# Performance work log

Hardware: AMD Instinct MI355X
Metric: run time of the kernel (lower is better)

The kernel has to match this reference:

```python
import jax, jax.numpy as jnp
import numpy as np

EPS = 1e-7
C_IN = 1.0
C_ATTN = 1.0
C_OUT = 1.0
B, N, D_IN, H, D_OUT = 4, 2048, 128, 8, 64  # in_features = D_IN+1, ambient A = D_OUT+1
INIT_BOUND = 0.02


def _lift(spatial, c):
    # lift spatial coords to hyperboloid of curvature c: x0 = sqrt(1/c + ||x_s||^2)
    time = jnp.sqrt(1.0 / c + jnp.sum(spatial * spatial, axis=-1, keepdims=True))
    return jnp.concatenate([time, spatial], axis=-1)


def _lorentz_normalize(mu, c):
    # project weighted sum back onto hyperboloid: mu / (sqrt(c) * sqrt(|<mu,mu>_L|))
    lor = -mu[..., 0:1] ** 2 + jnp.sum(mu[..., 1:] ** 2, axis=-1, keepdims=True)
    return mu / (jnp.sqrt(c) * jnp.sqrt(jnp.clip(-lor, EPS)))


def setup_inputs() -> dict:
    key = jax.random.key(0)
    ks = jax.random.split(key, 8)
    x_spatial = jax.random.normal(ks[0], (B, N, D_IN), dtype=jnp.float32) * 0.5
    x = _lift(x_spatial, C_IN)  # valid hyperboloid points, curvature C_IN
    u = lambda k, shp: jax.random.uniform(k, shp, minval=-INIT_BOUND, maxval=INIT_BOUND, dtype=jnp.float32)
    return {
        "x": x,
        "Wq": u(ks[1], (H, D_IN + 1, D_OUT)),
        "Wk": u(ks[2], (H, D_IN + 1, D_OUT)),
        "Wv": u(ks[3], (H, D_IN + 1, D_OUT)),
        "bq": u(ks[4], (H, D_OUT)),
        "bk": u(ks[5], (H, D_OUT)),
        "bv": u(ks[6], (H, D_OUT)),
        "scale": jnp.array(1.0, dtype=jnp.float32),
        "attn_bias": jnp.array(0.0, dtype=jnp.float32),
    }


def reference(x, Wq, Wk, Wv, bq, bk, bv, scale, attn_bias):
    # HTCLinear per head (vectorized over heads): spatial = x @ W + b, lift to curvature C_ATTN
    def proj(W, b):
        s = jnp.einsum('bni,hid->bnhd', x, W) + b  # (B,N,H,D_OUT)
        return _lift(s, C_ATTN)                    # (B,N,H,D_OUT+1)

    q = proj(Wq, bq)
    k = proj(Wk, bk)
    v = proj(Wv, bv)

    # Lorentzian inner product scores: -q0*k0 + q_s . k_s  -> (B,N,H,M)
    li = (-jnp.einsum('bnh,bmh->bnhm', q[..., 0], k[..., 0])
          + jnp.einsum('bnhd,bmhd->bnhm', q[..., 1:], k[..., 1:]))
    scores = (2.0 + 2.0 * li) / (scale + EPS) + attn_bias
    w = jax.nn.softmax(scores, axis=-1)

    # Lorentz midpoint aggregation over keys
    mu = jnp.einsum('bnhm,bmha->bnha', w, v)
    mid = _lorentz_normalize(mu, C_ATTN)  # (B,N,H,A)

    # uniform Lorentz midpoint over heads (weights 1/H)
    avg = jnp.mean(mid, axis=2)           # (B,N,A)
    out = _lorentz_normalize(avg, C_ATTN)

    # spatial_to_hyperboloid: rescale curvature C_ATTN -> C_OUT and re-lift
    spatial = out[..., 1:] * jnp.sqrt(C_ATTN / C_OUT)
    return _lift(spatial, C_OUT)  # (B,N,D_OUT+1)
```

## Files before the change

### kernel.cpp

```cpp
#include <hip/hip_runtime.h>
#include <hip/hip_bf16.h>

typedef __bf16 bf16x8 __attribute__((ext_vector_type(8)));
typedef float f32x16 __attribute__((ext_vector_type(16)));
typedef unsigned int u32;
typedef unsigned short u16;
typedef u32 u32x2 __attribute__((ext_vector_type(2)));
typedef u32 u32x4 __attribute__((ext_vector_type(4)));

static constexpr int Nn  = 2048;
static constexpr int DIN = 129;
static constexpr int QP  = 80;
static constexpr int AMB = 65;
static constexpr int XP  = 144;
static constexpr int NS  = 2;
static constexpr int PR  = 72;
static constexpr int KROW = 88;
static constexpr int KTS  = 3072;
static constexpr int VROW = 40;
static constexpr int VTS  = 4096;
static constexpr float LOG2E = 1.4426950408889634f;

#define DEV static __device__ __forceinline__

#if __has_builtin(__builtin_amdgcn_exp2f)
#define FEXP2 __builtin_amdgcn_exp2f
#else
#define FEXP2 exp2f
#endif

DEV u16 f2bf(float f) {
  union { __bf16 h; u16 u; } c;
  c.h = (__bf16)f;
  return c.u;
}
DEV float bf2f(u16 u) {
  union { float f; u32 uu; } c;
  c.uu = ((u32)u) << 16;
  return c.f;
}
DEV u32 cvtpk(float a, float b) {
  u32 r;
  asm("v_cvt_pk_bf16_f32 %0, %1, %2" : "=v"(r) : "v"(a), "v"(b));
  return r;
}
DEV void swap32(u32& a, u32& b) {
  asm("v_permlane32_swap_b32 %0, %1" : "+v"(a), "+v"(b));
}
DEV void gload_lds16(const u16* g, u16* l) {
  __builtin_amdgcn_global_load_lds(
      (const __attribute__((address_space(1))) unsigned int*)g,
      (__attribute__((address_space(3))) unsigned int*)l, 16, 0, 0);
}

__global__ __launch_bounds__(256) void prep_k(const float* __restrict__ x,
                                              u16* __restrict__ xb) {
  const int t = blockIdx.x * 256 + threadIdx.x;
  const int row = t / 18, cg = t % 18;
  u16 tmp[8];
#pragma unroll
  for (int j = 0; j < 8; ++j) {
    const int c = cg * 8 + j;
    tmp[j] = (c < DIN) ? f2bf(x[(size_t)row * DIN + c]) : (u16)0;
  }
  u32x4 w;
  w[0] = (u32)tmp[0] | ((u32)tmp[1] << 16);
  w[1] = (u32)tmp[2] | ((u32)tmp[3] << 16);
  w[2] = (u32)tmp[4] | ((u32)tmp[5] << 16);
  w[3] = (u32)tmp[6] | ((u32)tmp[7] << 16);
  *((u32x4*)xb + t) = w;
}

__global__ __launch_bounds__(256) void proj_k(
    const u16* __restrict__ xb,
    const float* __restrict__ Wq, const float* __restrict__ Wk, const float* __restrict__ Wv,
    const float* __restrict__ bq, const float* __restrict__ bk, const float* __restrict__ bv,
    const float* __restrict__ scale_p,
    u16* __restrict__ Qb, u16* __restrict__ Ktl, u16* __restrict__ Vtl) {
  __shared__ u16 wt[64][152];
  __shared__ __align__(16) u16 tiles[4][2816];

  const int tid = threadIdx.x;
  const int wid = tid >> 6, l = tid & 63;
  const int z = blockIdx.y;
  const int T = z >> 3, h = z & 7;
  const float* W    = (T == 0 ? Wq : (T == 1 ? Wk : Wv)) + (size_t)h * DIN * 64;
  const float* bias = (T == 0 ? bq : (T == 1 ? bk : bv)) + h * 64;

  {
    const int d = tid & 63, kk = tid >> 6;
    for (int k = kk; k < XP; k += 4)
      wt[d][k] = (k < DIN) ? f2bf(W[(size_t)k * 64 + d]) : (u16)0;
  }
  __syncthreads();

  const int lo = l & 31, hi = l >> 5;
  const int row0 = (blockIdx.x * 4 + wid) * 32;
  const u16* xr = xb + (size_t)(row0 + lo) * XP;

  f32x16 acc0 = {}, acc1 = {};
#pragma unroll
  for (int s = 0; s < 9; ++s) {
    bf16x8 a  = *(const bf16x8*)&xr[16 * s + 8 * hi];
    bf16x8 b0 = *(const bf16x8*)&wt[lo][16 * s + 8 * hi];
    bf16x8 b1 = *(const bf16x8*)&wt[32 + lo][16 * s + 8 * hi];
    acc0 = __builtin_amdgcn_mfma_f32_32x32x16_bf16(a, b0, acc0, 0, 0, 0);
    acc1 = __builtin_amdgcn_mfma_f32_32x32x16_bf16(a, b1, acc1, 0, 0, 0);
  }
  const float b0v = bias[lo], b1v = bias[32 + lo];
  const float alpha = 2.0f * LOG2E / (scale_p[0] + 1e-7f);
  u16* tl = &tiles[wid][0];

#pragma unroll
  for (int r = 0; r < 16; ++r) {
    const float s0 = acc0[r] + b0v;
    const float s1 = acc1[r] + b1v;
    float part = s0 * s0 + s1 * s1;
#pragma unroll
    for (int m = 1; m < 32; m <<= 1) part += __shfl_xor(part, m);
    const float time = sqrtf(1.0f + part);
    const int dr = (r & 3) + 8 * (r >> 2) + 4 * hi;
    if (T == 0) {
      tl[dr * 80 + lo]      = f2bf(alpha * s0);
      tl[dr * 80 + 32 + lo] = f2bf(alpha * s1);
      if (lo == 0) tl[dr * 80 + 64] = f2bf(alpha * time);
      if (lo < 15) tl[dr * 80 + 65 + lo] = 0;
    } else if (T == 1) {
      tl[dr * 88 + lo]      = f2bf(s0);
      tl[dr * 88 + 32 + lo] = f2bf(s1);
      if (lo == 0) tl[dr * 88 + 64] = f2bf(-(time - 1.0f));
      if (lo < 15) tl[dr * 88 + 65 + lo] = 0;
      if (lo < 8)  tl[dr * 88 + 80 + lo] = 0;
    } else {
      tl[lo * 40 + dr]        = f2bf(s0);
      tl[(32 + lo) * 40 + dr] = f2bf(s1);
      if (lo == 0) tl[64 * 40 + dr] = f2bf(time);
    }
  }
  __syncthreads();

  const int b = row0 >> 11, n0 = row0 & 2047;
  const int bh = b * 8 + h;
  u16* gdst;
  int nch;
  if (T == 0) { gdst = Qb + ((size_t)bh * Nn + n0) * QP;                nch = 320; }
  else if (T == 1) { gdst = Ktl + (size_t)bh * 64 * KTS + (size_t)(n0 >> 5) * KTS; nch = 352; }
  else { gdst = Vtl + (size_t)bh * 64 * VTS + (size_t)(n0 >> 5) * VTS;  nch = 325; }
  for (int j = l; j < nch; j += 64)
    *(u32x4*)(gdst + j * 8) = *(const u32x4*)(tl + j * 8);
}

DEV void stage_tile(const u16* kg, const u16* vg, u16* kl, u16* vl,
                    const int w, const int lane) {
  if (w < 2) {
#pragma unroll
    for (int i = 0; i < 3; ++i)
      gload_lds16(kg + (w * 3 + i) * 512 + lane * 8, kl + (w * 3 + i) * 512);
    gload_lds16(vg + w * 512 + lane * 8, vl + w * 512);
  } else {
#pragma unroll
    for (int i = 0; i < 3; ++i) {
      const int j = (w - 2) * 3 + 2 + i;
      gload_lds16(vg + j * 512 + lane * 8, vl + j * 512);
    }
  }
}

DEV void waitbar(const int w) {
  if (w < 2)
    asm volatile("s_waitcnt vmcnt(4) lgkmcnt(0)\ns_barrier" ::: "memory");
  else
    asm volatile("s_waitcnt vmcnt(3) lgkmcnt(0)\ns_barrier" ::: "memory");
}

DEV void exp_pack(const f32x16 sc, bf16x8& fA, bf16x8& fB) {
  float p[16];
#pragma unroll
  for (int r = 0; r < 16; ++r) p[r] = FEXP2(sc[r]);
  u32 a0 = cvtpk(p[0], p[1]),  a1 = cvtpk(p[2], p[3]);
  u32 a2 = cvtpk(p[4], p[5]),  a3 = cvtpk(p[6], p[7]);
  u32 c0 = cvtpk(p[8], p[9]),  c1 = cvtpk(p[10], p[11]);
  u32 c2 = cvtpk(p[12], p[13]), c3 = cvtpk(p[14], p[15]);
  swap32(a0, a2);
  swap32(a1, a3);
  swap32(c0, c2);
  swap32(c1, c3);
  union { u32x4 u; bf16x8 b; } ca, cb;
  ca.u = (u32x4){a0, a1, a2, a3};
  cb.u = (u32x4){c0, c1, c2, c3};
  fA = ca.b;
  fB = cb.b;
}

DEV void compute_tile64(const u16* kl, const u16* vl, const int lo, const int hi,
                        const bf16x8 (&qA)[5], const bf16x8 (&qB)[5],
                        f32x16& a0, f32x16& a1, f32x16& a2,
                        f32x16& b0, f32x16& b1, f32x16& b2) {
  f32x16 sA = {}, sB = {};
#pragma unroll
  for (int s = 0; s < 5; ++s) {
    const bf16x8 kf = *(const bf16x8*)&kl[lo * KROW + 16 * s + 8 * hi];
    sA = __builtin_amdgcn_mfma_f32_32x32x16_bf16(kf, qA[s], sA, 0, 0, 0);
    sB = __builtin_amdgcn_mfma_f32_32x32x16_bf16(kf, qB[s], sB, 0, 0, 0);
  }
  bf16x8 fA0, fB0, fA1, fB1;
  exp_pack(sA, fA0, fB0);
  exp_pack(sB, fA1, fB1);
#pragma unroll
  for (int t = 0; t < 3; ++t) {
    const bf16x8 va = *(const bf16x8*)&vl[(32 * t + lo) * VROW + 8 * hi];
    const bf16x8 vb = *(const bf16x8*)&vl[(32 * t + lo) * VROW + 16 + 8 * hi];
    f32x16& oa = (t == 0 ? a0 : (t == 1 ? a1 : a2));
    f32x16& ob = (t == 0 ? b0 : (t == 1 ? b1 : b2));
    oa = __builtin_amdgcn_mfma_f32_32x32x16_bf16(va, fA0, oa, 0, 0, 0);
    oa = __builtin_amdgcn_mfma_f32_32x32x16_bf16(vb, fB0, oa, 0, 0, 0);
    ob = __builtin_amdgcn_mfma_f32_32x32x16_bf16(va, fA1, ob, 0, 0, 0);
    ob = __builtin_amdgcn_mfma_f32_32x32x16_bf16(vb, fB1, ob, 0, 0, 0);
  }
}

DEV void write_partial(u16* part, const int bh, const int sidx, const int q,
                       const int hi, const f32x16& o0, const f32x16& o1,
                       const f32x16& o2) {
  u16* po = part + ((size_t)((bh * NS + sidx) * Nn + q)) * PR;
#pragma unroll
  for (int t = 0; t < 4; ++t) {
    const u32 a0 = cvtpk(o0[4 * t], o0[4 * t + 1]);
    const u32 a1 = cvtpk(o0[4 * t + 2], o0[4 * t + 3]);
    const u32 b0 = cvtpk(o1[4 * t], o1[4 * t + 1]);
    const u32 b1 = cvtpk(o1[4 * t + 2], o1[4 * t + 3]);
    *(u32x2*)&po[8 * t + 4 * hi]      = (u32x2){a0, a1};
    *(u32x2*)&po[8 * t + 4 * hi + 32] = (u32x2){b0, b1};
  }
  if (hi == 0) po[64] = f2bf(o2[0]);
}

__global__ __launch_bounds__(256, 2) void attn_k(
    const u16* __restrict__ Qb, const u16* __restrict__ Ktl,
    const u16* __restrict__ Vtl, u16* __restrict__ part) {
  __shared__ u16 kls[3][KTS];
  __shared__ u16 vls[3][VTS];

  const int tid  = threadIdx.x;
  const int w    = tid >> 6, lane = tid & 63;
  const int lo   = lane & 31, hi = lane >> 5;

  const u32 bid = blockIdx.x;
  const u32 swz = (bid & 7) * 64 + (bid >> 3);
  const int bh   = swz >> 4;
  const int sidx = (swz >> 3) & 1;
  const int qt   = swz & 7;
  const int qbase = qt * 256 + w * 64;

  const u16* qrowA = Qb + ((size_t)bh * Nn + qbase + lo) * QP;
  const u16* qrowB = qrowA + 32 * QP;
  bf16x8 qA[5], qB[5];
#pragma unroll
  for (int s = 0; s < 5; ++s) {
    qA[s] = *(const bf16x8*)&qrowA[16 * s + 8 * hi];
    qB[s] = *(const bf16x8*)&qrowB[16 * s + 8 * hi];
  }

  f32x16 a0 = {}, a1 = {}, a2 = {};
  f32x16 b0 = {}, b1 = {}, b2 = {};
  const u16* ktb = Ktl + (size_t)bh * 64 * KTS + (size_t)(sidx * 32) * KTS;
  const u16* vtb = Vtl + (size_t)bh * 64 * VTS + (size_t)(sidx * 32) * VTS;

  stage_tile(ktb, vtb, kls[0], vls[0], w, lane);
  stage_tile(ktb + KTS, vtb + VTS, kls[1], vls[1], w, lane);
  waitbar(w);

#pragma unroll 1
  for (int t = 0; t < 32; ++t) {
    const int pf = (t + 2 < 32) ? t + 2 : 31;
    stage_tile(ktb + (size_t)pf * KTS, vtb + (size_t)pf * VTS,
               kls[(t + 2) % 3], vls[(t + 2) % 3], w, lane);
    compute_tile64(kls[t % 3], vls[t % 3], lo, hi, qA, qB, a0, a1, a2, b0, b1, b2);
    waitbar(w);
  }

  write_partial(part, bh, sidx, qbase + lo,      hi, a0, a1, a2);
  write_partial(part, bh, sidx, qbase + 32 + lo, hi, b0, b1, b2);
}

__global__ __launch_bounds__(256) void finale_k(const u16* __restrict__ part,
                                                float* __restrict__ out) {
  const int tid = threadIdx.x;
  const int wv = tid >> 6, l = tid & 63;
  const int g = blockIdx.x * 4 + wv;
  const int b = g >> 11, n = g & 2047;
  const int h = l >> 3, c = l & 7;

  const u16* rowp = part + ((size_t)((b * 8 + h) * NS) * Nn + n) * PR;
  float Oh[8];
#pragma unroll
  for (int j = 0; j < 8; ++j) Oh[j] = 0.f;
  float th = 0.f;
#pragma unroll
  for (int s = 0; s < NS; ++s) {
    const u16* rp = rowp + (size_t)s * Nn * PR;
    const u32x4 v = *(const u32x4*)&rp[8 * c];
#pragma unroll
    for (int i = 0; i < 4; ++i) {
      union { u32 u; float f; } a, bb;
      a.u  = v[i] << 16;
      bb.u = v[i] & 0xffff0000u;
      Oh[2 * i]     += a.f;
      Oh[2 * i + 1] += bb.f;
    }
    th += bf2f(rp[64]);
  }

  float sq = 0.f;
#pragma unroll
  for (int j = 0; j < 8; ++j) sq += Oh[j] * Oh[j];
  sq += __shfl_xor(sq, 1);
  sq += __shfl_xor(sq, 2);
  sq += __shfl_xor(sq, 4);
  const float invh = rsqrtf(fmaxf(th * th - sq, 1e-7f));

  float S[8];
#pragma unroll
  for (int j = 0; j < 8; ++j) S[j] = Oh[j] * invh;
  float T = th * invh;
#pragma unroll
  for (int m = 8; m <= 32; m <<= 1) {
#pragma unroll
    for (int j = 0; j < 8; ++j) S[j] += __shfl_xor(S[j], m);
    T += __shfl_xor(T, m);
  }

  float s2 = 0.f;
#pragma unroll
  for (int j = 0; j < 8; ++j) s2 += S[j] * S[j];
  s2 += __shfl_xor(s2, 1);
  s2 += __shfl_xor(s2, 2);
  s2 += __shfl_xor(s2, 4);
  const float inv = rsqrtf(fmaxf(T * T - s2, 1e-7f));
  const float ssp = s2 * inv * inv;

  float* o = out + (size_t)g * AMB;
  if (h == 0) {
#pragma unroll
    for (int j = 0; j < 8; ++j) o[1 + 8 * c + j] = S[j] * inv;
    if (l == 0) o[0] = sqrtf(1.0f + ssp);
  }
}

extern "C" void kernel_launch(void* const* d_in, const int* in_sizes, int n_in,
                              void* d_out, int out_size, void* d_ws, size_t ws_size,
                              hipStream_t stream) {
  (void)in_sizes; (void)n_in; (void)out_size; (void)ws_size;
  const float* x  = (const float*)d_in[0];
  const float* Wq = (const float*)d_in[1];
  const float* Wk = (const float*)d_in[2];
  const float* Wv = (const float*)d_in[3];
  const float* bq = (const float*)d_in[4];
  const float* bk = (const float*)d_in[5];
  const float* bv = (const float*)d_in[6];
  const float* sc = (const float*)d_in[7];

  char* ws = (char*)d_ws;
  u16*  Qb  = (u16*)(ws);
  u16*  Ktl = (u16*)(ws + 10485760);
  u16*  Vtl = (u16*)(ws + 23068672);
  u16*  pb  = (u16*)(ws + 39845888);
  u16*  xb  = (u16*)(ws + 39845888);
  float* out = (float*)d_out;

  hipLaunchKernelGGL(prep_k, dim3(576), dim3(256), 0, stream, x, xb);
  hipLaunchKernelGGL(proj_k, dim3(64, 24), dim3(256), 0, stream,
                     xb, Wq, Wk, Wv, bq, bk, bv, sc, Qb, Ktl, Vtl);
  hipLaunchKernelGGL(attn_k, dim3(512), dim3(256), 0, stream, Qb, Ktl, Vtl, pb);
  hipLaunchKernelGGL(finale_k, dim3(2048), dim3(256), 0, stream, pb, out);
}
```

Before: 102.2 us.

## Fold bias into projection GEMM, transpose MFMA output, and double-buffer 2-tile superstages

The projection kernel now folds the bias into the GEMM by appending a constant 1 column to x and a bias row to W. It also swaps the MFMA operands so each lane holds a whole row, which turns the 5-step shuffle reduction per element into a single cross-half shuffle and allows packed vector stores to LDS. The attention kernel replaces its triple-buffered single-tile pipeline with double-buffered 2-tile superstages: half as many barriers, but each stage now waits with vmcnt(0) and so loses some prefetch depth. LDS per block rises from 3 to 4 tiles' worth, which may affect occupancy at 2 blocks per CU.

```diff
diff --git a/kernel.cpp b/kernel.cpp
--- a/kernel.cpp
+++ b/kernel.cpp
@@ -61,7 +61,8 @@
 #pragma unroll
   for (int j = 0; j < 8; ++j) {
     const int c = cg * 8 + j;
-    tmp[j] = (c < DIN) ? f2bf(x[(size_t)row * DIN + c]) : (u16)0;
+    tmp[j] = (c < DIN) ? f2bf(x[(size_t)row * DIN + c])
+                       : (c == DIN ? f2bf(1.0f) : (u16)0);
   }
   u32x4 w;
   w[0] = (u32)tmp[0] | ((u32)tmp[1] << 16);
@@ -90,7 +91,8 @@
   {
     const int d = tid & 63, kk = tid >> 6;
     for (int k = kk; k < XP; k += 4)
-      wt[d][k] = (k < DIN) ? f2bf(W[(size_t)k * 64 + d]) : (u16)0;
+      wt[d][k] = (k < DIN) ? f2bf(W[(size_t)k * 64 + d])
+                           : (k == DIN ? f2bf(bias[d]) : (u16)0);
   }
   __syncthreads();
 
@@ -104,38 +106,50 @@
     bf16x8 a  = *(const bf16x8*)&xr[16 * s + 8 * hi];
     bf16x8 b0 = *(const bf16x8*)&wt[lo][16 * s + 8 * hi];
     bf16x8 b1 = *(const bf16x8*)&wt[32 + lo][16 * s + 8 * hi];
-    acc0 = __builtin_amdgcn_mfma_f32_32x32x16_bf16(a, b0, acc0, 0, 0, 0);
-    acc1 = __builtin_amdgcn_mfma_f32_32x32x16_bf16(a, b1, acc1, 0, 0, 0);
-  }
-  const float b0v = bias[lo], b1v = bias[32 + lo];
+    acc0 = __builtin_amdgcn_mfma_f32_32x32x16_bf16(b0, a, acc0, 0, 0, 0);
+    acc1 = __builtin_amdgcn_mfma_f32_32x32x16_bf16(b1, a, acc1, 0, 0, 0);
+  }
   const float alpha = 2.0f * LOG2E / (scale_p[0] + 1e-7f);
+
+  float nrm = 0.f;
+#pragma unroll
+  for (int r = 0; r < 16; ++r) nrm += acc0[r] * acc0[r] + acc1[r] * acc1[r];
+  nrm += __shfl_xor(nrm, 32);
+  const float time = sqrtf(1.0f + nrm);
+
   u16* tl = &tiles[wid][0];
-
-#pragma unroll
-  for (int r = 0; r < 16; ++r) {
-    const float s0 = acc0[r] + b0v;
-    const float s1 = acc1[r] + b1v;
-    float part = s0 * s0 + s1 * s1;
-#pragma unroll
-    for (int m = 1; m < 32; m <<= 1) part += __shfl_xor(part, m);
-    const float time = sqrtf(1.0f + part);
-    const int dr = (r & 3) + 8 * (r >> 2) + 4 * hi;
-    if (T == 0) {
-      tl[dr * 80 + lo]      = f2bf(alpha * s0);
-      tl[dr * 80 + 32 + lo] = f2bf(alpha * s1);
-      if (lo == 0) tl[dr * 80 + 64] = f2bf(alpha * time);
-      if (lo < 15) tl[dr * 80 + 65 + lo] = 0;
-    } else if (T == 1) {
-      tl[dr * 88 + lo]      = f2bf(s0);
-      tl[dr * 88 + 32 + lo] = f2bf(s1);
-      if (lo == 0) tl[dr * 88 + 64] = f2bf(-(time - 1.0f));
-      if (lo < 15) tl[dr * 88 + 65 + lo] = 0;
-      if (lo < 8)  tl[dr * 88 + 80 + lo] = 0;
-    } else {
-      tl[lo * 40 + dr]        = f2bf(s0);
-      tl[(32 + lo) * 40 + dr] = f2bf(s1);
-      if (lo == 0) tl[64 * 40 + dr] = f2bf(time);
+  if (T == 0) {
+#pragma unroll
+    for (int g = 0; g < 4; ++g) {
+      const u32 w0 = cvtpk(alpha * acc0[4 * g],     alpha * acc0[4 * g + 1]);
+      const u32 w1 = cvtpk(alpha * acc0[4 * g + 2], alpha * acc0[4 * g + 3]);
+      const u32 w2 = cvtpk(alpha * acc1[4 * g],     alpha * acc1[4 * g + 1]);
+      const u32 w3 = cvtpk(alpha * acc1[4 * g + 2], alpha * acc1[4 * g + 3]);
+      *(u32x2*)&tl[lo * 80 + 8 * g + 4 * hi]      = (u32x2){w0, w1};
+      *(u32x2*)&tl[lo * 80 + 32 + 8 * g + 4 * hi] = (u32x2){w2, w3};
     }
+    if (hi == 0) *(u32x4*)&tl[lo * 80 + 64] = (u32x4){(u32)f2bf(alpha * time), 0, 0, 0};
+    else         *(u32x4*)&tl[lo * 80 + 72] = (u32x4){0, 0, 0, 0};
+  } else if (T == 1) {
+#pragma unroll
+    for (int g = 0; g < 4; ++g) {
+      const u32 w0 = cvtpk(acc0[4 * g],     acc0[4 * g + 1]);
+      const u32 w1 = cvtpk(acc0[4 * g + 2], acc0[4 * g + 3]);
+      const u32 w2 = cvtpk(acc1[4 * g],     acc1[4 * g + 1]);
+      const u32 w3 = cvtpk(acc1[4 * g + 2], acc1[4 * g + 3]);
+      *(u32x2*)&tl[lo * 88 + 8 * g + 4 * hi]      = (u32x2){w0, w1};
+      *(u32x2*)&tl[lo * 88 + 32 + 8 * g + 4 * hi] = (u32x2){w2, w3};
+    }
+    if (hi == 0) *(u32x4*)&tl[lo * 88 + 64] = (u32x4){(u32)f2bf(-(time - 1.0f)), 0, 0, 0};
+    else         *(u32x4*)&tl[lo * 88 + 72] = (u32x4){0, 0, 0, 0};
+  } else {
+#pragma unroll
+    for (int r = 0; r < 16; ++r) {
+      const int d = (r & 3) + 8 * (r >> 2) + 4 * hi;
+      tl[d * 40 + lo]        = f2bf(acc0[r]);
+      tl[(32 + d) * 40 + lo] = f2bf(acc1[r]);
+    }
+    if (hi == 0) tl[64 * 40 + lo] = f2bf(time);
   }
   __syncthreads();
 
@@ -150,27 +164,27 @@
     *(u32x4*)(gdst + j * 8) = *(const u32x4*)(tl + j * 8);
 }
 
-DEV void stage_tile(const u16* kg, const u16* vg, u16* kl, u16* vl,
-                    const int w, const int lane) {
-  if (w < 2) {
-#pragma unroll
-    for (int i = 0; i < 3; ++i)
-      gload_lds16(kg + (w * 3 + i) * 512 + lane * 8, kl + (w * 3 + i) * 512);
-    gload_lds16(vg + w * 512 + lane * 8, vl + w * 512);
+DEV void stage_super(const u16* kg, const u16* vg, u16* kl, u16* vl,
+                     const int w, const int lane) {
+  if (w == 0) {
+#pragma unroll
+    for (int i = 0; i < 6; ++i) gload_lds16(kg + i * 512 + lane * 8, kl + i * 512);
+    gload_lds16(vg + lane * 8, vl);
+  } else if (w == 1) {
+#pragma unroll
+    for (int i = 1; i < 8; ++i) gload_lds16(vg + i * 512 + lane * 8, vl + i * 512);
+  } else if (w == 2) {
+#pragma unroll
+    for (int i = 6; i < 12; ++i) gload_lds16(kg + i * 512 + lane * 8, kl + i * 512);
+    gload_lds16(vg + 8 * 512 + lane * 8, vl + 8 * 512);
   } else {
 #pragma unroll
-    for (int i = 0; i < 3; ++i) {
-      const int j = (w - 2) * 3 + 2 + i;
-      gload_lds16(vg + j * 512 + lane * 8, vl + j * 512);
-    }
-  }
-}
-
-DEV void waitbar(const int w) {
-  if (w < 2)
-    asm volatile("s_waitcnt vmcnt(4) lgkmcnt(0)\ns_barrier" ::: "memory");
-  else
-    asm volatile("s_waitcnt vmcnt(3) lgkmcnt(0)\ns_barrier" ::: "memory");
+    for (int i = 9; i < 16; ++i) gload_lds16(vg + i * 512 + lane * 8, vl + i * 512);
+  }
+}
+
+DEV void waitbar() {
+  asm volatile("s_waitcnt vmcnt(0) lgkmcnt(0)\ns_barrier" ::: "memory");
 }
 
 DEV void exp_pack(const f32x16 sc, bf16x8& fA, bf16x8& fB) {
@@ -238,8 +252,8 @@
 __global__ __launch_bounds__(256, 2) void attn_k(
     const u16* __restrict__ Qb, const u16* __restrict__ Ktl,
     const u16* __restrict__ Vtl, u16* __restrict__ part) {
-  __shared__ u16 kls[3][KTS];
-  __shared__ u16 vls[3][VTS];
+  __shared__ u16 kls[2][2 * KTS];
+  __shared__ u16 vls[2][2 * VTS];
 
   const int tid  = threadIdx.x;
   const int w    = tid >> 6, lane = tid & 63;
@@ -266,17 +280,17 @@
   const u16* ktb = Ktl + (size_t)bh * 64 * KTS + (size_t)(sidx * 32) * KTS;
   const u16* vtb = Vtl + (size_t)bh * 64 * VTS + (size_t)(sidx * 32) * VTS;
 
-  stage_tile(ktb, vtb, kls[0], vls[0], w, lane);
-  stage_tile(ktb + KTS, vtb + VTS, kls[1], vls[1], w, lane);
-  waitbar(w);
+  stage_super(ktb, vtb, kls[0], vls[0], w, lane);
+  waitbar();
 
 #pragma unroll 1
-  for (int t = 0; t < 32; ++t) {
-    const int pf = (t + 2 < 32) ? t + 2 : 31;
-    stage_tile(ktb + (size_t)pf * KTS, vtb + (size_t)pf * VTS,
-               kls[(t + 2) % 3], vls[(t + 2) % 3], w, lane);
-    compute_tile64(kls[t % 3], vls[t % 3], lo, hi, qA, qB, a0, a1, a2, b0, b1, b2);
-    waitbar(w);
+  for (int s = 0; s < 16; ++s) {
+    const int pf = (s + 1 < 16) ? s + 1 : 15;
+    stage_super(ktb + (size_t)pf * 2 * KTS, vtb + (size_t)pf * 2 * VTS,
+                kls[(s + 1) & 1], vls[(s + 1) & 1], w, lane);
+    compute_tile64(kls[s & 1],       vls[s & 1],       lo, hi, qA, qB, a0, a1, a2, b0, b1, b2);
+    compute_tile64(kls[s & 1] + KTS, vls[s & 1] + VTS, lo, hi, qA, qB, a0, a1, a2, b0, b1, b2);
+    waitbar();
   }
 
   write_partial(part, bh, sidx, qbase + lo,      hi, a0, a1, a2);
```

Result: faster. 93.23 us (-8.8%).
